# Kernel tuning notes

Measured on AMD Instinct MI355X. Metric: run time of the kernel, lower is better.

The kernel has to match this reference:

```python
import jax, jax.numpy as jnp
import numpy as np

H = 12          # num attention heads
D = 768         # hidden size
DH = D // H     # head dim = 64

def setup_inputs() -> dict:
    key = jax.random.key(0)
    ks = jax.random.split(key, 9)
    B, N = 8, 1024
    s = 0.02
    return {
        "hidden_states": jax.random.normal(ks[0], (B, N, D), jnp.float32),
        "Wq": jax.random.normal(ks[1], (D, D), jnp.float32) * s,
        "bq": jnp.zeros((D,), jnp.float32),
        "Wk": jax.random.normal(ks[2], (D, D), jnp.float32) * s,
        "bk": jnp.zeros((D,), jnp.float32),
        "Wv": jax.random.normal(ks[3], (D, D), jnp.float32) * s,
        "bv": jnp.zeros((D,), jnp.float32),
        "Wo": jax.random.normal(ks[4], (D, D), jnp.float32) * s,
        "bo": jnp.zeros((D,), jnp.float32),
    }

def _split_heads(x):
    # [B, N, D] -> [B, H, N, DH]
    B, N, _ = x.shape
    return x.reshape(B, N, H, DH).transpose(0, 2, 1, 3)

def reference(hidden_states, Wq, bq, Wk, bk, Wv, bv, Wo, bo):
    # torch Linear: y = x @ W.T + b
    q = _split_heads(hidden_states @ Wq.T + bq)
    k = _split_heads(hidden_states @ Wk.T + bk)
    v = _split_heads(hidden_states @ Wv.T + bv)
    scale = 1.0 / jnp.sqrt(jnp.asarray(DH, hidden_states.dtype))
    scores = jnp.einsum("bhqd,bhkd->bhqk", q, k) * scale
    probs = jax.nn.softmax(scores, axis=-1)
    ctx = jnp.einsum("bhqk,bhkd->bhqd", probs, v)
    B, _, N, _ = ctx.shape
    ctx = ctx.transpose(0, 2, 1, 3).reshape(B, N, D)
    return ctx @ Wo.T + bo
```

## Files before the change

kernel.cpp:

```cpp
#include <hip/hip_runtime.h>

typedef unsigned short u16;
typedef unsigned int   u32;
typedef unsigned long long u64;
typedef __attribute__((ext_vector_type(8))) short bf16x8;
typedef __attribute__((ext_vector_type(4))) float f32x4;
typedef __attribute__((address_space(3))) u32 lds_u32;
typedef __attribute__((address_space(1))) u32 gbl_u32;

#define MFMA16(a,b,c) __builtin_amdgcn_mfma_f32_16x16x32_bf16((a),(b),(c),0,0,0)
#define QSCALE 0.1803368801111204f

#define WAIT5 do{ asm volatile("s_waitcnt vmcnt(5)" ::: "memory"); }while(0)
#define WAIT4 do{ asm volatile("s_waitcnt vmcnt(4)" ::: "memory"); }while(0)
#define WAIT0 do{ asm volatile("s_waitcnt vmcnt(0)" ::: "memory"); }while(0)
#define SCHED __builtin_amdgcn_sched_barrier(0)
#define BARR  __builtin_amdgcn_s_barrier()

__device__ __forceinline__ u16 f2bf(float f){
  u32 u = __builtin_bit_cast(u32, f);
  u32 r = u + 0x7fffu + ((u>>16)&1u);
  return (u16)(r>>16);
}
__device__ __forceinline__ float bf2f(u16 h){
  return __builtin_bit_cast(float, (u32)h<<16);
}

union V8 { u16 s[8]; uint4 v; };

__global__ __launch_bounds__(256) void cvt_all(const float* __restrict__ hs,
    const float* __restrict__ Wq, const float* __restrict__ Wk,
    const float* __restrict__ Wv, const float* __restrict__ Wo,
    u16* __restrict__ hsb, u16* __restrict__ wqkv, u16* __restrict__ woh)
{
  const int bid = blockIdx.x;
  if (bid < 3072){
    int i = bid*256 + threadIdx.x;
    const float4* p = (const float4*)(hs + (size_t)i*8);
    float4 a = p[0], b = p[1];
    V8 t;
    t.s[0]=f2bf(a.x); t.s[1]=f2bf(a.y); t.s[2]=f2bf(a.z); t.s[3]=f2bf(a.w);
    t.s[4]=f2bf(b.x); t.s[5]=f2bf(b.y); t.s[6]=f2bf(b.z); t.s[7]=f2bf(b.w);
    *(uint4*)(hsb + (size_t)i*8) = t.v;
    return;
  }
  const int r = bid - 3072;
  const int seg = r / 288;
  const int off = (r - seg*288)*256 + threadIdx.x;
  const float* src = seg==0?Wq: seg==1?Wk: seg==2?Wv: Wo;
  const float4* p = (const float4*)(src + (size_t)off*8);
  float4 a = p[0], b = p[1];
  float xs[8] = {a.x,a.y,a.z,a.w,b.x,b.y,b.z,b.w};
  V8 t;
  #pragma unroll
  for (int j=0;j<8;++j) t.s[j]=f2bf(xs[j]);
  if (seg < 3) *(uint4*)(wqkv + (size_t)seg*589824 + (size_t)off*8) = t.v;
  else         *(uint4*)(woh  + (size_t)off*8) = t.v;
}

__global__ __launch_bounds__(256) void mm_qkv(const u16* __restrict__ A, const u16* __restrict__ Bp,
    const float* __restrict__ bq, const float* __restrict__ bk, const float* __restrict__ bvv,
    u16* __restrict__ Oq, u16* __restrict__ Ok, u16* __restrict__ Ov)
{
  __shared__ u16 P[3][10240];
  const int bid = blockIdx.x;
  const int sid = (bid & 7)*96 + (bid >> 3);
  const int mb = sid/12, nb = sid - mb*12;
  const int m0 = mb*128, n0 = nb*192;
  const int tid = threadIdx.x;
  const int lane = tid&63, wid = tid>>6;
  const int wr = wid>>1, wc = wid&1;
  const int fr = lane&15, fg = lane>>4;

  const char* Ab = (const char*)A;
  const char* Bb = (const char*)Bp;
  const char* sp[5];
  #pragma unroll
  for (int c=0;c<5;++c){
    int ci = c*256 + tid;
    if (ci < 512){
      int line = ci>>3, slot = ci&7;
      int d = slot ^ (line&7);
      int row = 2*line + (d>>2);
      sp[c] = Ab + (size_t)(m0+row)*1536 + (d&3)*16;
    } else {
      int i = ci - 512;
      int line = i>>3, slot = i&7;
      int d = slot ^ (line&7);
      int row = 2*line + (d>>2);
      sp[c] = Bb + (size_t)(n0+row)*1536 + (d&3)*16;
    }
  }
  const int sl = (((fr&1)<<2) + fg) ^ (fr>>1);
  const int aoff = (fr&~1)*64 + sl*16 + wr*4096;
  const int boff = 8192 + (fr&~1)*64 + sl*16 + wc*6144;

  f32x4 zz = {0.f,0.f,0.f,0.f};
  f32x4 acc[4][6];
  #pragma unroll
  for (int i=0;i<4;++i)
    #pragma unroll
    for (int j=0;j<6;++j) acc[i][j]=zz;

  auto STAGE = [&](int t, int b){
    char* dst0 = (char*)P[b];
    #pragma unroll
    for (int c=0;c<5;++c)
      __builtin_amdgcn_global_load_lds((const gbl_u32*)(sp[c] + (size_t)t*64),
        (lds_u32*)(dst0 + c*4096 + tid*16), 16, 0, 0);
  };
  auto COMPUTE = [&](int b){
    const char* pb = (const char*)P[b];
    bf16x8 bfr[6];
    #pragma unroll
    for (int nt=0;nt<6;++nt)
      bfr[nt] = *(const bf16x8*)(pb + boff + nt*1024);
    #pragma unroll
    for (int mt=0;mt<4;++mt){
      bf16x8 af = *(const bf16x8*)(pb + aoff + mt*1024);
      #pragma unroll
      for (int nt=0;nt<6;++nt)
        acc[mt][nt] = MFMA16(af, bfr[nt], acc[mt][nt]);
    }
  };

  STAGE(0, 0); STAGE(1, 1);
  int cb = 0;
  for (int t=0; t<24; ++t){
    if (t < 23) WAIT5; else WAIT0;
    BARR; SCHED;
    if (t < 22){
      int sb = cb + 2; if (sb >= 3) sb -= 3;
      STAGE(t+2, sb);
    }
    __builtin_amdgcn_s_setprio(1);
    COMPUTE(cb);
    __builtin_amdgcn_s_setprio(0);
    cb = (cb == 2) ? 0 : cb + 1;
  }

  const int seg = nb/4;
  const float* bias = seg==0?bq: seg==1?bk:bvv;
  const float sc = (seg==0) ? QSCALE : 1.0f;
  if (seg < 2){
    u16* O = seg==0?Oq:Ok;
    #pragma unroll
    for (int mt=0;mt<4;++mt){
      #pragma unroll
      for (int nt=0;nt<6;++nt){
        int colw = n0 + wc*96 + nt*16 + fr - seg*768;
        float bz = bias[colw];
        int hh = colw>>6, d = colw&63;
        #pragma unroll
        for (int rr=0;rr<4;++rr){
          int row = m0 + wr*64 + mt*16 + fg*4 + rr;
          int b = row>>10, nn = row&1023;
          O[((size_t)(b*12+hh)<<16) + (size_t)nn*64 + d] = f2bf((acc[mt][nt][rr] + bz) * sc);
        }
      }
    }
  } else {
    #pragma unroll
    for (int mt=0;mt<4;++mt){
      #pragma unroll
      for (int nt=0;nt<6;++nt){
        int colw = n0 + wc*96 + nt*16 + fr - 1536;
        float bz = bias[colw];
        int hh = colw>>6, d = colw&63;
        int row0 = m0 + wr*64 + mt*16 + fg*4;
        int b = row0>>10, nn = row0&1023;
        union { u16 h[4]; u64 q; } pk;
        #pragma unroll
        for (int rr=0;rr<4;++rr) pk.h[rr] = f2bf(acc[mt][nt][rr] + bz);
        *(u64*)&Ov[((size_t)(b*12+hh)<<16) + (size_t)d*1024 + nn] = pk.q;
      }
    }
  }
}

__global__ __launch_bounds__(256) void mm_o(const u16* __restrict__ A, const u16* __restrict__ Bp,
                                            const float* __restrict__ bias, float* __restrict__ O)
{
  __shared__ u16 P[3][8192];
  const int bid = blockIdx.x;
  const int sid = (bid & 7)*48 + (bid >> 3);
  const int mb = sid/6, nb = sid - mb*6;
  const int m0 = mb*128, n0 = nb*128;
  const int tid = threadIdx.x;
  const int lane = tid&63, wid = tid>>6;
  const int wr = wid>>1, wc = wid&1;
  const int fr = lane&15, fg = lane>>4;

  const char* Ab = (const char*)A;
  const char* Bb = (const char*)Bp;
  const char* sp[4];
  #pragma unroll
  for (int c=0;c<4;++c){
    int ci = c*256 + tid;
    int row = ci>>3, slot = ci&7;
    int d = slot ^ (row&7);
    if (d < 4) sp[c] = Ab + (size_t)(m0+row)*1536 + d*16;
    else       sp[c] = Bb + (size_t)(n0+row)*1536 + (d-4)*16;
  }
  const int sA = (fg ^ (fr&7)) << 4;
  const int sB = sA ^ 64;

  f32x4 zz = {0.f,0.f,0.f,0.f};
  f32x4 acc[4][4];
  #pragma unroll
  for (int i=0;i<4;++i)
    #pragma unroll
    for (int j=0;j<4;++j) acc[i][j]=zz;

  auto STAGE = [&](int t, int b){
    char* dst0 = (char*)P[b];
    #pragma unroll
    for (int c=0;c<4;++c)
      __builtin_amdgcn_global_load_lds((const gbl_u32*)(sp[c] + (size_t)t*64),
        (lds_u32*)(dst0 + c*4096 + wid*1024), 16, 0, 0);
  };
  auto COMPUTE = [&](int b){
    const char* pb = (const char*)P[b];
    bf16x8 bfr[4];
    #pragma unroll
    for (int nt=0;nt<4;++nt)
      bfr[nt] = *(const bf16x8*)(pb + (wc*64+nt*16+fr)*128 + sB);
    #pragma unroll
    for (int mt=0;mt<4;++mt){
      bf16x8 af = *(const bf16x8*)(pb + (wr*64+mt*16+fr)*128 + sA);
      #pragma unroll
      for (int nt=0;nt<4;++nt)
        acc[mt][nt] = MFMA16(af, bfr[nt], acc[mt][nt]);
    }
  };

  STAGE(0, 0); STAGE(1, 1);
  int cb = 0;
  for (int t=0; t<24; ++t){
    if (t < 23) WAIT4; else WAIT0;
    BARR; SCHED;
    if (t < 22){
      int sb = cb + 2; if (sb >= 3) sb -= 3;
      STAGE(t+2, sb);
    }
    __builtin_amdgcn_s_setprio(1);
    COMPUTE(cb);
    __builtin_amdgcn_s_setprio(0);
    cb = (cb == 2) ? 0 : cb + 1;
  }

  #pragma unroll
  for (int mt=0;mt<4;++mt){
    #pragma unroll
    for (int nt=0;nt<4;++nt){
      int colb = n0 + wc*64 + nt*16 + fr;
      float bz = bias[colb];
      #pragma unroll
      for (int rr=0;rr<4;++rr){
        int row = m0 + wr*64 + mt*16 + fg*4 + rr;
        O[(size_t)row*768 + colb] = acc[mt][nt][rr] + bz;
      }
    }
  }
}

__global__ __launch_bounds__(256, 2) void attn(const u16* __restrict__ qh, const u16* __restrict__ kh,
                                               const u16* __restrict__ vh, u16* __restrict__ ch)
{
  __shared__ u16 Kb[2][4096];
  __shared__ u16 Vb[2][4096];
  __shared__ u16 Ps[4][64][72];
  const int tid=threadIdx.x, w=tid>>6, lane=tid&63;
  const int fr=lane&15, fg=lane>>4;
  const int bh=blockIdx.x, qt=blockIdx.y;
  const size_t base=(size_t)bh<<16;
  const int q0=qt*256 + w*64;

  const char* kbase = (const char*)(kh + base);
  const char* vbase = (const char*)(vh + base);

  int koff[2], voff[2];
  #pragma unroll
  for (int c=0;c<2;++c){
    int ci = c*256 + tid;
    int row = ci>>3;
    int colp = ((ci&7)*16) ^ ((row&7)<<4);
    koff[c] = row*128  + colp;
    voff[c] = row*2048 + colp;
  }

  bf16x8 qf[4][2];
  #pragma unroll
  for (int mt=0;mt<4;++mt)
    #pragma unroll
    for (int ks=0;ks<2;++ks)
      qf[mt][ks] = *(const bf16x8*)&qh[base + (size_t)(q0+mt*16+fr)*64 + ks*32 + fg*8];

  const int swz = (fr&7)<<4;
  int lowD[2];
  #pragma unroll
  for (int ks=0;ks<2;++ks) lowD[ks] = (ks*64 + fg*16) ^ swz;
  const int frbase = fr*128;

  const short one_bf = (short)0x3F80;
  bf16x8 ones = {one_bf,one_bf,one_bf,one_bf,one_bf,one_bf,one_bf,one_bf};

  f32x4 zz = {0.f,0.f,0.f,0.f};
  f32x4 o[4][4];
  f32x4 ol[4];
  #pragma unroll
  for (int mt=0;mt<4;++mt){
    ol[mt]=zz;
    #pragma unroll
    for (int j=0;j<4;++j) o[mt][j]=zz;
  }

  {
    #pragma unroll
    for (int c=0;c<2;++c){
      __builtin_amdgcn_global_load_lds((const gbl_u32*)(kbase + koff[c]),
        (lds_u32*)((char*)&Kb[0][0] + c*4096 + w*1024), 16, 0, 0);
      __builtin_amdgcn_global_load_lds((const gbl_u32*)(vbase + voff[c]),
        (lds_u32*)((char*)&Vb[0][0] + c*4096 + w*1024), 16, 0, 0);
    }
  }
  __syncthreads();

  for (int kt=0; kt<16; ++kt){
    const int buf = kt & 1;
    {
      const int ktn = (kt+1) & 15;
      const char* kt_ = kbase + ktn*8192;
      const char* vt_ = vbase + ktn*128;
      #pragma unroll
      for (int c=0;c<2;++c){
        __builtin_amdgcn_global_load_lds((const gbl_u32*)(kt_ + koff[c]),
          (lds_u32*)((char*)&Kb[buf^1][0] + c*4096 + w*1024), 16, 0, 0);
        __builtin_amdgcn_global_load_lds((const gbl_u32*)(vt_ + voff[c]),
          (lds_u32*)((char*)&Vb[buf^1][0] + c*4096 + w*1024), 16, 0, 0);
      }
    }

    f32x4 s[4][4];
    #pragma unroll
    for (int mt=0;mt<4;++mt)
      #pragma unroll
      for (int j=0;j<4;++j) s[mt][j]=zz;
    const char* kb = (const char*)&Kb[buf][0];
    __builtin_amdgcn_s_setprio(1);
    #pragma unroll
    for (int ct=0;ct<4;++ct){
      #pragma unroll
      for (int ks=0;ks<2;++ks){
        bf16x8 kf = *(const bf16x8*)(kb + ct*2048 + frbase + lowD[ks]);
        #pragma unroll
        for (int mt=0;mt<4;++mt)
          s[mt][ct]=MFMA16(kf,qf[mt][ks],s[mt][ct]);
      }
    }
    __builtin_amdgcn_s_setprio(0);

    #pragma unroll
    for (int mt=0;mt<4;++mt){
      #pragma unroll
      for (int ct=0;ct<4;++ct){
        float e0 = __builtin_amdgcn_exp2f(s[mt][ct][0]);
        float e1 = __builtin_amdgcn_exp2f(s[mt][ct][1]);
        float e2 = __builtin_amdgcn_exp2f(s[mt][ct][2]);
        float e3 = __builtin_amdgcn_exp2f(s[mt][ct][3]);
        u32 w0, w1;
        asm("v_cvt_pk_bf16_f32 %0, %1, %2" : "=v"(w0) : "v"(e0), "v"(e1));
        asm("v_cvt_pk_bf16_f32 %0, %1, %2" : "=v"(w1) : "v"(e2), "v"(e3));
        uint2 pk2; pk2.x = w0; pk2.y = w1;
        *(uint2*)&Ps[w][mt*16+fr][ct*16+fg*4] = pk2;
      }
    }

    const char* vb = (const char*)&Vb[buf][0];
    __builtin_amdgcn_s_setprio(1);
    #pragma unroll
    for (int ks2=0;ks2<2;++ks2){
      bf16x8 vf[4];
      #pragma unroll
      for (int dt=0;dt<4;++dt)
        vf[dt] = *(const bf16x8*)(vb + dt*2048 + frbase + lowD[ks2]);
      #pragma unroll
      for (int mt=0;mt<4;++mt){
        bf16x8 pa = *(const bf16x8*)&Ps[w][mt*16+fr][ks2*32+fg*8];
        #pragma unroll
        for (int dt=0;dt<4;++dt)
          o[mt][dt]=MFMA16(pa, vf[dt], o[mt][dt]);
        ol[mt]=MFMA16(pa, ones, ol[mt]);
      }
    }
    __builtin_amdgcn_s_setprio(0);

    __syncthreads();
  }

  const int b=bh/12, hd=bh%12;
  #pragma unroll
  for (int mt=0;mt<4;++mt){
    float inv[4];
    #pragma unroll
    for (int rr=0;rr<4;++rr) inv[rr] = 1.0f / ol[mt][rr];
    #pragma unroll
    for (int dt=0;dt<4;++dt){
      int d = dt*16 + fr;
      #pragma unroll
      for (int rr=0;rr<4;++rr){
        int n = q0 + mt*16 + fg*4 + rr;
        ch[((size_t)b*1024 + n)*768 + hd*64 + d] = f2bf(o[mt][dt][rr] * inv[rr]);
      }
    }
  }
}

extern "C" void kernel_launch(void* const* d_in, const int* in_sizes, int n_in,
                              void* d_out, int out_size, void* d_ws, size_t ws_size,
                              hipStream_t stream) {
  const float* hs = (const float*)d_in[0];
  const float* Wq = (const float*)d_in[1];
  const float* bq = (const float*)d_in[2];
  const float* Wk = (const float*)d_in[3];
  const float* bk = (const float*)d_in[4];
  const float* Wv = (const float*)d_in[5];
  const float* bv = (const float*)d_in[6];
  const float* Wo = (const float*)d_in[7];
  const float* bo = (const float*)d_in[8];
  float* out = (float*)d_out;

  const size_t PS = (size_t)8192*768;
  u16* ws16  = (u16*)d_ws;
  u16* hs_bf = ws16;
  u16* q_bf  = ws16 + PS;
  u16* k_bf  = ws16 + 2*PS;
  u16* v_bf  = ws16 + 3*PS;
  u16* wqkv  = ws16 + 4*PS;
  u16* woh   = wqkv + 3*589824;
  u16* c_hi  = hs_bf;

  dim3 blk(256);
  cvt_all<<<3072 + 4*288, blk, 0, stream>>>(hs, Wq, Wk, Wv, Wo, hs_bf, wqkv, woh);
  mm_qkv<<<768, blk, 0, stream>>>(hs_bf, wqkv, bq, bk, bv, q_bf, k_bf, v_bf);
  attn<<<dim3(96,4), blk, 0, stream>>>(q_bf, k_bf, v_bf, c_hi);
  mm_o<<<384, blk, 0, stream>>>(c_hi, woh, bo, out);
}
```

Before: 110.2 us.

## Use 512-thread blocks in QKV GEMM with 2x4 wave tiling

The QKV projection GEMM now runs with 8 waves per block instead of 4. Each wave computes a 64x48 tile rather than 64x96, which halves the accumulator registers per wave. The global-to-LDS staging loads are redistributed across 512 threads, with the upper four waves issuing one fewer load, and the vmcnt waits are adjusted per wave. The aim is more latency hiding and MFMA issue parallelism per CU, at the cost of each wave reusing its A fragments across fewer B columns, so more LDS reads per MFMA.

```diff
diff --git a/kernel.cpp b/kernel.cpp
--- a/kernel.cpp
+++ b/kernel.cpp
@@ -11,7 +11,8 @@
 #define MFMA16(a,b,c) __builtin_amdgcn_mfma_f32_16x16x32_bf16((a),(b),(c),0,0,0)
 #define QSCALE 0.1803368801111204f
 
-#define WAIT5 do{ asm volatile("s_waitcnt vmcnt(5)" ::: "memory"); }while(0)
+#define WAIT3 do{ asm volatile("s_waitcnt vmcnt(3)" ::: "memory"); }while(0)
+#define WAIT2 do{ asm volatile("s_waitcnt vmcnt(2)" ::: "memory"); }while(0)
 #define WAIT4 do{ asm volatile("s_waitcnt vmcnt(4)" ::: "memory"); }while(0)
 #define WAIT0 do{ asm volatile("s_waitcnt vmcnt(0)" ::: "memory"); }while(0)
 #define SCHED __builtin_amdgcn_sched_barrier(0)
@@ -58,7 +59,7 @@
   else         *(uint4*)(woh  + (size_t)off*8) = t.v;
 }
 
-__global__ __launch_bounds__(256) void mm_qkv(const u16* __restrict__ A, const u16* __restrict__ Bp,
+__global__ __launch_bounds__(512) void mm_qkv(const u16* __restrict__ A, const u16* __restrict__ Bp,
     const float* __restrict__ bq, const float* __restrict__ bk, const float* __restrict__ bvv,
     u16* __restrict__ Oq, u16* __restrict__ Ok, u16* __restrict__ Ov)
 {
@@ -69,57 +70,66 @@
   const int m0 = mb*128, n0 = nb*192;
   const int tid = threadIdx.x;
   const int lane = tid&63, wid = tid>>6;
-  const int wr = wid>>1, wc = wid&1;
+  const int wm = wid>>2, wn = wid&3;
   const int fr = lane&15, fg = lane>>4;
+  const int nst = (wid<4) ? 3 : 2;
 
   const char* Ab = (const char*)A;
   const char* Bb = (const char*)Bp;
-  const char* sp[5];
-  #pragma unroll
-  for (int c=0;c<5;++c){
-    int ci = c*256 + tid;
+  const char* sp[3];
+  int ldst[3];
+  #pragma unroll
+  for (int c=0;c<3;++c){
+    int ci = c*512 + tid;
+    if (c==2) ci = 1024 + tid;
     if (ci < 512){
       int line = ci>>3, slot = ci&7;
       int d = slot ^ (line&7);
       int row = 2*line + (d>>2);
       sp[c] = Ab + (size_t)(m0+row)*1536 + (d&3)*16;
-    } else {
+    } else if (ci < 1280){
       int i = ci - 512;
       int line = i>>3, slot = i&7;
       int d = slot ^ (line&7);
       int row = 2*line + (d>>2);
       sp[c] = Bb + (size_t)(n0+row)*1536 + (d&3)*16;
-    }
-  }
+    } else {
+      sp[c] = Ab;
+    }
+    ldst[c] = ci*16;
+  }
+
   const int sl = (((fr&1)<<2) + fg) ^ (fr>>1);
-  const int aoff = (fr&~1)*64 + sl*16 + wr*4096;
-  const int boff = 8192 + (fr&~1)*64 + sl*16 + wc*6144;
+  const int aoff = (fr&~1)*64 + sl*16 + wm*4096;
+  const int boff = 8192 + (fr&~1)*64 + sl*16 + wn*3072;
 
   f32x4 zz = {0.f,0.f,0.f,0.f};
-  f32x4 acc[4][6];
+  f32x4 acc[4][3];
   #pragma unroll
   for (int i=0;i<4;++i)
     #pragma unroll
-    for (int j=0;j<6;++j) acc[i][j]=zz;
+    for (int j=0;j<3;++j) acc[i][j]=zz;
 
   auto STAGE = [&](int t, int b){
     char* dst0 = (char*)P[b];
     #pragma unroll
-    for (int c=0;c<5;++c)
+    for (int c=0;c<3;++c){
+      if (c==2 && wid>=4) break;
       __builtin_amdgcn_global_load_lds((const gbl_u32*)(sp[c] + (size_t)t*64),
-        (lds_u32*)(dst0 + c*4096 + tid*16), 16, 0, 0);
+        (lds_u32*)(dst0 + ldst[c]), 16, 0, 0);
+    }
   };
   auto COMPUTE = [&](int b){
     const char* pb = (const char*)P[b];
-    bf16x8 bfr[6];
-    #pragma unroll
-    for (int nt=0;nt<6;++nt)
+    bf16x8 bfr[3];
+    #pragma unroll
+    for (int nt=0;nt<3;++nt)
       bfr[nt] = *(const bf16x8*)(pb + boff + nt*1024);
     #pragma unroll
     for (int mt=0;mt<4;++mt){
       bf16x8 af = *(const bf16x8*)(pb + aoff + mt*1024);
       #pragma unroll
-      for (int nt=0;nt<6;++nt)
+      for (int nt=0;nt<3;++nt)
         acc[mt][nt] = MFMA16(af, bfr[nt], acc[mt][nt]);
     }
   };
@@ -127,7 +137,7 @@
   STAGE(0, 0); STAGE(1, 1);
   int cb = 0;
   for (int t=0; t<24; ++t){
-    if (t < 23) WAIT5; else WAIT0;
+    if (t < 23){ if (wid < 4) WAIT3; else WAIT2; } else WAIT0;
     BARR; SCHED;
     if (t < 22){
       int sb = cb + 2; if (sb >= 3) sb -= 3;
@@ -147,13 +157,13 @@
     #pragma unroll
     for (int mt=0;mt<4;++mt){
       #pragma unroll
-      for (int nt=0;nt<6;++nt){
-        int colw = n0 + wc*96 + nt*16 + fr - seg*768;
+      for (int nt=0;nt<3;++nt){
+        int colw = n0 + wn*48 + nt*16 + fr - seg*768;
         float bz = bias[colw];
         int hh = colw>>6, d = colw&63;
         #pragma unroll
         for (int rr=0;rr<4;++rr){
-          int row = m0 + wr*64 + mt*16 + fg*4 + rr;
+          int row = m0 + wm*64 + mt*16 + fg*4 + rr;
           int b = row>>10, nn = row&1023;
           O[((size_t)(b*12+hh)<<16) + (size_t)nn*64 + d] = f2bf((acc[mt][nt][rr] + bz) * sc);
         }
@@ -163,11 +173,11 @@
     #pragma unroll
     for (int mt=0;mt<4;++mt){
       #pragma unroll
-      for (int nt=0;nt<6;++nt){
-        int colw = n0 + wc*96 + nt*16 + fr - 1536;
+      for (int nt=0;nt<3;++nt){
+        int colw = n0 + wn*48 + nt*16 + fr - 1536;
         float bz = bias[colw];
         int hh = colw>>6, d = colw&63;
-        int row0 = m0 + wr*64 + mt*16 + fg*4;
+        int row0 = m0 + wm*64 + mt*16 + fg*4;
         int b = row0>>10, nn = row0&1023;
         union { u16 h[4]; u64 q; } pk;
         #pragma unroll
@@ -442,7 +452,7 @@
 
   dim3 blk(256);
   cvt_all<<<3072 + 4*288, blk, 0, stream>>>(hs, Wq, Wk, Wv, Wo, hs_bf, wqkv, woh);
-  mm_qkv<<<768, blk, 0, stream>>>(hs_bf, wqkv, bq, bk, bv, q_bf, k_bf, v_bf);
+  mm_qkv<<<768, dim3(512), 0, stream>>>(hs_bf, wqkv, bq, bk, bv, q_bf, k_bf, v_bf);
   attn<<<dim3(96,4), blk, 0, stream>>>(q_bf, k_bf, v_bf, c_hi);
   mm_o<<<384, blk, 0, stream>>>(c_hi, woh, bo, out);
 }
```

Result: no change. 110.4 us (+0.2%).
